# Optimization experiments

Hardware: AMD Instinct MI355X
Metric: run time of the kernel (lower is better)

Reference implementation:

```python
import jax, jax.numpy as jnp
import numpy as np

B, N, H = 32, 1024, 128
EPS = 1e-5


def setup_inputs() -> dict:
    key = jax.random.key(0)
    ks = jax.random.split(key, 9)
    node_embeddings = jax.random.normal(ks[0], (B, N, H), dtype=jnp.float32)
    edge_relations = jax.random.normal(ks[1], (B, N, N, 3), dtype=jnp.float32)
    adjacency = jax.random.randint(ks[2], (N, N), 0, 2, dtype=jnp.int32)
    s_msg = 1.0 / np.sqrt(H + 3)
    s_upd = 1.0 / np.sqrt(2 * H)
    W_msg = jax.random.uniform(ks[3], (H, H + 3), jnp.float32, -s_msg, s_msg)
    b_msg = jax.random.uniform(ks[4], (H,), jnp.float32, -s_msg, s_msg)
    W_upd = jax.random.uniform(ks[5], (H, 2 * H), jnp.float32, -s_upd, s_upd)
    b_upd = jax.random.uniform(ks[6], (H,), jnp.float32, -s_upd, s_upd)
    gamma = jnp.ones((H,), jnp.float32)
    beta = jnp.zeros((H,), jnp.float32)
    return {"node_embeddings": node_embeddings, "edge_relations": edge_relations,
            "adjacency": adjacency, "W_msg": W_msg, "b_msg": b_msg,
            "W_upd": W_upd, "b_upd": b_upd, "gamma": gamma, "beta": beta}


def reference(node_embeddings, edge_relations, adjacency, W_msg, b_msg, W_upd, b_upd, gamma, beta):
    # node_embeddings: [B,N,H]; edge_relations: [B,N,N,3]; adjacency: [N,N]
    b_, n_, h_ = node_embeddings.shape
    mask = (adjacency > 0).astype(node_embeddings.dtype)  # mask[j,i]=1 if i is neighbor of j
    # Split msg_nn weight: Linear(cat(h_i, e_ij)) = h_i @ W_h^T + e_ij @ W_e^T + b
    W_h = W_msg[:, :h_]   # [H,H]
    W_e = W_msg[:, h_:]   # [H,3]
    h_part = jnp.einsum('bih,oh->bio', node_embeddings, W_h)       # [B,N,H]
    msg_h = jnp.einsum('ji,bio->bjo', mask, h_part)                # aggregate sender linear part
    e_agg = jnp.einsum('bijc,ji->bjc', edge_relations, mask)       # aggregate edge feats first (memory-bound)
    msg_e = jnp.einsum('bjc,oc->bjo', e_agg, W_e)
    deg = mask.sum(axis=1)                                         # [N] in-degree of j
    messages = msg_h + msg_e + deg[None, :, None] * b_msg          # bias added once per edge
    # Dropout(0.2) is identity in inference; BatchNorm uses batch stats (training-mode math).
    upd_in = jnp.concatenate([node_embeddings, messages], axis=-1)  # [B,N,2H]
    updated = jax.nn.relu(jnp.einsum('bjk,ok->bjo', upd_in, W_upd) + b_upd)
    flat = updated.reshape(-1, h_)
    mean = flat.mean(axis=0)
    var = flat.var(axis=0)  # biased, as BatchNorm1d
    normed = (flat - mean) * jax.lax.rsqrt(var + EPS) * gamma + beta
    return normed.reshape(b_, n_, h_) + node_embeddings
```

## Files before the change

### kernel.cpp

```cpp
#include <hip/hip_runtime.h>

typedef _Float16 f16;
typedef f16 f16x4 __attribute__((ext_vector_type(4)));
typedef f16 f16x8 __attribute__((ext_vector_type(8)));
typedef float f32x4 __attribute__((ext_vector_type(4)));

#define BB 32
#define NN 1024
#define HH 128
#define ROWS (BB*NN)
#define EPS 1e-5f

__device__ __forceinline__ f16 f2h(float x) { return (f16)x; }

typedef __attribute__((address_space(1))) const void gv_t;
typedef __attribute__((address_space(3))) void lv_t;
__device__ __forceinline__ void gl_lds16(const void* g, void* l) {
  __builtin_amdgcn_global_load_lds((gv_t*)g, (lv_t*)l, 16, 0, 0);
}

__global__ __launch_bounds__(256) void prep0_k(
    const float* __restrict__ W_msg, const float* __restrict__ W_upd,
    const float* __restrict__ node, const int* __restrict__ adj,
    f16* __restrict__ Wh, f16* __restrict__ Wupd, float* __restrict__ We,
    f16* __restrict__ nodeh, f16* __restrict__ maskf, f16* __restrict__ maskT,
    float* __restrict__ e_agg, float* __restrict__ sums)
{
  const int blk = blockIdx.x, t = threadIdx.x;
  if (blk < 64) {
    const long base = (long)blk*16384 + t;
    #pragma unroll
    for (int p = 0; p < 64; p++) {
      const long idx = base + (long)p*256;
      const float4 v = ((const float4*)node)[idx];
      f16x4 hv; hv[0] = f2h(v.x); hv[1] = f2h(v.y); hv[2] = f2h(v.z); hv[3] = f2h(v.w);
      *(f16x4*)&nodeh[idx << 2] = hv;
    }
  } else if (blk < 128) {
    __shared__ f16 ldsT[128][136];
    const int tt = blk - 64, tj = tt >> 3, ti = tt & 7;
    #pragma unroll
    for (int p = 0; p < 16; p++) {
      const int q = p*256 + t;
      const int row = q >> 5, c4 = (q & 31) << 2;
      const int4 m = *(const int4*)&adj[(long)(tj*128 + row)*NN + ti*128 + c4];
      f16x4 hv;
      hv[0] = (m.x > 0) ? (f16)1.0f : (f16)0.0f;
      hv[1] = (m.y > 0) ? (f16)1.0f : (f16)0.0f;
      hv[2] = (m.z > 0) ? (f16)1.0f : (f16)0.0f;
      hv[3] = (m.w > 0) ? (f16)1.0f : (f16)0.0f;
      *(f16x4*)&maskf[(long)(tj*128 + row)*NN + ti*128 + c4] = hv;
      ldsT[c4 + 0][row] = hv[0];
      ldsT[c4 + 1][row] = hv[1];
      ldsT[c4 + 2][row] = hv[2];
      ldsT[c4 + 3][row] = hv[3];
    }
    __syncthreads();
    #pragma unroll
    for (int p = 0; p < 8; p++) {
      const int q = p*256 + t;
      const int rT = q >> 4, c8 = (q & 15) << 3;
      *(uint4*)&maskT[(long)(ti*128 + rT)*NN + tj*128 + c8] =
          *(const uint4*)&ldsT[rT][c8];
    }
  } else if (blk == 128) {
    for (int idx = t; idx < HH*HH; idx += 256) {
      const int o = idx >> 7, h = idx & 127;
      Wh[idx] = f2h(W_msg[o*131 + h]);
    }
  } else if (blk == 129) {
    for (int idx = t; idx < HH*256; idx += 256)
      Wupd[idx] = f2h(W_upd[idx]);
  } else if (blk == 130) {
    for (int idx = t; idx < HH*3; idx += 256)
      We[idx] = W_msg[(idx/3)*131 + 128 + (idx % 3)];
    if (t < 256) sums[t] = 0.f;
  } else {
    const int base = (blk - 131) * 24576 + t;
    #pragma unroll
    for (int r = 0; r < 96; r++) e_agg[base + r*256] = 0.f;
  }
}

__global__ __launch_bounds__(256) void phaseB_k(
    const f16* __restrict__ nodeh, const float* __restrict__ E,
    const f16* __restrict__ maskT, const f16* __restrict__ Wh,
    const float* __restrict__ b_msg,
    f16* __restrict__ h_part_T, float* __restrict__ e_agg)
{
  __shared__ __align__(16) char smem[24576];
  const int tid = threadIdx.x;

  if (blockIdx.x >= 256) {
    float* Ebuf = (float*)smem;
    const int e  = blockIdx.x - 256;
    const int bb = e >> 6;
    const int r6 = e & 63;
    const int jt = r6 & 3;
    const int ih = r6 >> 2;
    const int j  = (jt << 8) + tid;
    const int i0 = ih << 6;
    const int lane = tid & 63, wv = tid >> 6;
    const float* Eblk = E + (long)bb*3145728 + (long)i0*3072 + (long)(jt << 8)*3;
    float a0 = 0.f, a1 = 0.f, a2 = 0.f;
    for (int ch = 0; ch < 8; ch++) {
      const float* Ech = Eblk + (long)ch*8*3072;
      __syncthreads();
      #pragma unroll
      for (int k = 0; k < 6; k++) {
        const int m = wv*6 + k;
        const int r = m/3;
        const int cb = (m % 3) << 8;
        gl_lds16(Ech + (long)r*3072 + cb + lane*4, Ebuf + m*256);
      }
      float mreg[8];
      #pragma unroll
      for (int v = 0; v < 8; v++)
        mreg[v] = (float)maskT[(long)(i0 + ch*8 + v)*NN + j];
      __syncthreads();
      #pragma unroll
      for (int v = 0; v < 8; v++) {
        const float e0 = Ebuf[v*768 + tid*3];
        const float e1 = Ebuf[v*768 + tid*3 + 1];
        const float e2 = Ebuf[v*768 + tid*3 + 2];
        a0 = fmaf(mreg[v], e0, a0);
        a1 = fmaf(mreg[v], e1, a1);
        a2 = fmaf(mreg[v], e2, a2);
      }
    }
    const long eb = ((long)bb*NN + j)*3;
    atomicAdd(&e_agg[eb],     a0);
    atomicAdd(&e_agg[eb + 1], a1);
    atomicAdd(&e_agg[eb + 2], a2);
    return;
  }

  f16* As = (f16*)smem;
  f16* Bs = (f16*)(smem + 8192);
  const int g  = blockIdx.x;
  const int nt = g & 7, bb = g >> 3;
  const int nbase = nt << 7;
  const int lane = tid & 63, wave = tid >> 6;
  const int wm = (wave & 1) << 6, wn = (wave >> 1) << 6;

  f32x4 acc[2][4], acc2[2][4];
  #pragma unroll
  for (int i = 0; i < 2; i++)
    #pragma unroll
    for (int j = 0; j < 4; j++)
      #pragma unroll
      for (int r = 0; r < 4; r++) { acc[i][j][r] = 0.f; acc2[i][j][r] = 0.f; }

  for (int k0 = 0; k0 < HH; k0 += 32) {
    #pragma unroll
    for (int p = 0; p < 2; p++) {
      const int q = (p << 8) + tid;
      const int row = q >> 2, kp = (q & 3) << 3;
      gl_lds16(&Wh[(long)row*HH + k0 + kp], &As[q << 3]);
      gl_lds16(&nodeh[(long)((bb << 10) + nbase + row)*HH + k0 + kp], &Bs[q << 3]);
    }
    __syncthreads();
    f16x8 af[4], bf[4];
    #pragma unroll
    for (int i = 0; i < 4; i++) {
      af[i] = *(const f16x8*)&As[((wm + (i << 4) + (lane & 15)) << 5) + ((lane >> 4) << 3)];
      bf[i] = *(const f16x8*)&Bs[((wn + (i << 4) + (lane & 15)) << 5) + ((lane >> 4) << 3)];
    }
    #pragma unroll
    for (int i = 0; i < 2; i++)
      #pragma unroll
      for (int j = 0; j < 4; j++) {
        acc[i][j]  = __builtin_amdgcn_mfma_f32_16x16x32_f16(af[i],     bf[j], acc[i][j],  0, 0, 0);
        acc2[i][j] = __builtin_amdgcn_mfma_f32_16x16x32_f16(af[i + 2], bf[j], acc2[i][j], 0, 0, 0);
      }
    __syncthreads();
  }

  f16* out = h_part_T + (long)bb * (HH*NN);
  const int rb = (lane >> 4) << 2, cb = lane & 15;
  #pragma unroll
  for (int i = 0; i < 4; i++)
    #pragma unroll
    for (int r = 0; r < 4; r++) {
      const int gm = wm + (i << 4) + rb + r;
      const float bm = b_msg[gm];
      #pragma unroll
      for (int j = 0; j < 4; j++) {
        const int gn = nbase + wn + (j << 4) + cb;
        const float v = ((i < 2) ? acc[i][j][r] : acc2[i - 2][j][r]) + bm;
        out[(long)gm*NN + gn] = f2h(v);
      }
    }
}

__global__ __launch_bounds__(256) void gemm12_k(
    const f16* __restrict__ maskf, const f16* __restrict__ hp,
    const float* __restrict__ e_agg, const float* __restrict__ We,
    const f16* __restrict__ nodeh, const f16* __restrict__ Wupd,
    const float* __restrict__ b_upd,
    f16* __restrict__ upd, float* __restrict__ sums)
{
  const int mt = blockIdx.x, bb = blockIdx.z;
  const int jb = mt << 7;
  const long rowb = (long)bb*NN + jb;
  __shared__ f16 As[128*32];
  __shared__ f16 Bs[128*32];
  __shared__ __align__(16) char msgs_lds[128*128*2];
  __shared__ float colS[128], colQ[128];
  const int tid = threadIdx.x, lane = tid & 63, wave = tid >> 6;
  const int wm = (wave & 1) << 6, wn = (wave >> 1) << 6;
  if (tid < 128) { colS[tid] = 0.f; colQ[tid] = 0.f; }
  const int rb = (lane >> 4) << 2, cb = lane & 15;

  f32x4 acc[4][4];
  #pragma unroll
  for (int i = 0; i < 4; i++)
    #pragma unroll
    for (int j = 0; j < 4; j++)
      #pragma unroll
      for (int r = 0; r < 4; r++) acc[i][j][r] = 0.f;

  for (int k0 = 0; k0 < NN; k0 += 32) {
    #pragma unroll
    for (int p = 0; p < 2; p++) {
      const int q = (p << 8) + tid;
      const int row = q >> 2, kp = (q & 3) << 3;
      gl_lds16(&maskf[(long)(jb + row)*NN + k0 + kp], &As[q << 3]);
      gl_lds16(&hp[(long)bb*(HH*NN) + (long)row*NN + k0 + kp], &Bs[q << 3]);
    }
    __syncthreads();
    f16x8 af[4], bf[4];
    #pragma unroll
    for (int i = 0; i < 4; i++) {
      af[i] = *(const f16x8*)&As[((wm + (i << 4) + (lane & 15)) << 5) + ((lane >> 4) << 3)];
      bf[i] = *(const f16x8*)&Bs[((wn + (i << 4) + (lane & 15)) << 5) + ((lane >> 4) << 3)];
    }
    #pragma unroll
    for (int i = 0; i < 4; i++)
      #pragma unroll
      for (int j = 0; j < 4; j++)
        acc[i][j] = __builtin_amdgcn_mfma_f32_16x16x32_f16(af[i], bf[j], acc[i][j], 0, 0, 0);
    __syncthreads();
  }

  #pragma unroll
  for (int i = 0; i < 4; i++)
    #pragma unroll
    for (int r = 0; r < 4; r++) {
      const int lrow = wm + (i << 4) + rb + r;
      const long eb = (rowb + lrow)*3;
      const float e0 = e_agg[eb], e1 = e_agg[eb+1], e2 = e_agg[eb+2];
      #pragma unroll
      for (int j = 0; j < 4; j++) {
        const int col = wn + (j << 4) + cb;
        const float v = acc[i][j][r]
                      + e0*We[col*3] + e1*We[col*3+1] + e2*We[col*3+2];
        const int byte = ((lrow << 8) + (col << 1)) ^ ((lrow & 7) << 4);
        *(f16*)(msgs_lds + byte) = f2h(v);
      }
    }
  __syncthreads();

  f32x4 acc2[4][4];
  #pragma unroll
  for (int i = 0; i < 4; i++)
    #pragma unroll
    for (int j = 0; j < 4; j++)
      #pragma unroll
      for (int r = 0; r < 4; r++) acc2[i][j][r] = 0.f;

  for (int k0 = 0; k0 < 256; k0 += 32) {
    const bool fromA = (k0 < HH);
    #pragma unroll
    for (int p = 0; p < 2; p++) {
      const int q = (p << 8) + tid;
      const int row = q >> 2, kp = (q & 3) << 3;
      if (fromA)
        gl_lds16(&nodeh[(rowb + row)*HH + k0 + kp], &As[q << 3]);
      gl_lds16(&Wupd[(long)row*256 + k0 + kp], &Bs[q << 3]);
    }
    __syncthreads();
    f16x8 af[4], bf[4];
    #pragma unroll
    for (int i = 0; i < 4; i++) {
      if (fromA) {
        af[i] = *(const f16x8*)&As[((wm + (i << 4) + (lane & 15)) << 5) + ((lane >> 4) << 3)];
      } else {
        const int lrow = wm + (i << 4) + (lane & 15);
        const int byte = ((lrow << 8) + (((k0 - HH) + ((lane >> 4) << 3)) << 1))
                         ^ ((lrow & 7) << 4);
        af[i] = *(const f16x8*)(msgs_lds + byte);
      }
      bf[i] = *(const f16x8*)&Bs[((wn + (i << 4) + (lane & 15)) << 5) + ((lane >> 4) << 3)];
    }
    #pragma unroll
    for (int i = 0; i < 4; i++)
      #pragma unroll
      for (int j = 0; j < 4; j++)
        acc2[i][j] = __builtin_amdgcn_mfma_f32_16x16x32_f16(af[i], bf[j], acc2[i][j], 0, 0, 0);
    __syncthreads();
  }

  float bup[4], s[4] = {0,0,0,0}, qq[4] = {0,0,0,0};
  #pragma unroll
  for (int j = 0; j < 4; j++) bup[j] = b_upd[wn + (j << 4) + cb];
  #pragma unroll
  for (int i = 0; i < 4; i++)
    #pragma unroll
    for (int r = 0; r < 4; r++) {
      const long gm = rowb + wm + (i << 4) + rb + r;
      #pragma unroll
      for (int j = 0; j < 4; j++) {
        const int gn = wn + (j << 4) + cb;
        const float v = fmaxf(acc2[i][j][r] + bup[j], 0.f);
        upd[gm*HH + gn] = f2h(v);
        s[j] += v; qq[j] += v*v;
      }
    }
  #pragma unroll
  for (int j = 0; j < 4; j++) {
    const int gn = wn + (j << 4) + cb;
    atomicAdd(&colS[gn], s[j]);
    atomicAdd(&colQ[gn], qq[j]);
  }
  __syncthreads();
  if (tid < 128) {
    atomicAdd(&sums[tid],       colS[tid]);
    atomicAdd(&sums[128 + tid], colQ[tid]);
  }
}

__global__ __launch_bounds__(256) void final_k(const f16* __restrict__ upd,
    const float* __restrict__ node, const float* __restrict__ sums,
    const float* __restrict__ gamma, const float* __restrict__ beta,
    float* __restrict__ out)
{
  const long idx = (long)blockIdx.x*256 + threadIdx.x;
  const f16x4 u  = *(const f16x4*)&upd[idx << 2];
  const float4 nd = ((const float4*)node)[idx];
  const int ob = (idx & 31) << 2;
  const float inv = 1.0f/32768.0f;
  float4 res;
  #pragma unroll
  for (int c = 0; c < 4; c++) {
    const float m  = sums[ob + c]*inv;
    const float va = sums[128 + ob + c]*inv - m*m;
    const float sc = rsqrtf(va + EPS)*gamma[ob + c];
    ((float*)&res)[c] = ((float)u[c] - m)*sc + beta[ob + c]
                      + ((const float*)&nd)[c];
  }
  ((float4*)out)[idx] = res;
}

extern "C" void kernel_launch(void* const* d_in, const int* in_sizes, int n_in,
                              void* d_out, int out_size, void* d_ws, size_t ws_size,
                              hipStream_t stream) {
  const float* node  = (const float*)d_in[0];
  const float* E     = (const float*)d_in[1];
  const int*   adj   = (const int*)  d_in[2];
  const float* W_msg = (const float*)d_in[3];
  const float* b_msg = (const float*)d_in[4];
  const float* W_upd = (const float*)d_in[5];
  const float* b_upd = (const float*)d_in[6];
  const float* gamma = (const float*)d_in[7];
  const float* beta  = (const float*)d_in[8];
  float* out = (float*)d_out;

  char* p = (char*)d_ws;
  auto alloc = [&](size_t n) { void* r = (void*)p; p += (n + 255) & ~(size_t)255; return r; };
  f16*   h_part_T = (f16*)  alloc((size_t)BB*HH*NN*2);
  f16*   upd      = (f16*)  alloc((size_t)ROWS*HH*2);
  f16*   nodeh    = (f16*)  alloc((size_t)ROWS*HH*2);
  f16*   maskf    = (f16*)  alloc((size_t)NN*NN*2);
  f16*   maskT    = (f16*)  alloc((size_t)NN*NN*2);
  float* e_agg    = (float*)alloc((size_t)BB*NN*3*4);
  f16*   Wh       = (f16*)  alloc((size_t)HH*HH*2);
  f16*   Wupd     = (f16*)  alloc((size_t)HH*256*2);
  float* We       = (float*)alloc((size_t)HH*3*4);
  float* sums     = (float*)alloc((size_t)256*4);

  prep0_k<<<135, 256, 0, stream>>>(W_msg, W_upd, node, adj,
                                   Wh, Wupd, We, nodeh, maskf, maskT,
                                   e_agg, sums);

  phaseB_k<<<2304, 256, 0, stream>>>(nodeh, E, maskT, Wh, b_msg, h_part_T, e_agg);

  gemm12_k<<<dim3(8, 1, BB), 256, 0, stream>>>(maskf, h_part_T, e_agg, We,
                                               nodeh, Wupd, b_upd, upd, sums);

  final_k<<<4096, 256, 0, stream>>>(upd, node, sums, gamma, beta, out);
}
```

Before: 630.7 us.

## Stream edge features with direct float4 loads instead of LDS staging

The edge-aggregation blocks in phaseB now read edge_relations with per-thread float4 loads straight into registers. This replaces the global-to-LDS staging and the two barriers per chunk. Each thread covers four consecutive floats that can span two destination nodes, so it selects between two mask values per component. Work is re-split into 3072 smaller blocks of 32 rows each, which means more atomics to e_agg, and shared memory shrinks because the LDS buffer is gone.

```diff
diff --git a/kernel.cpp b/kernel.cpp
--- a/kernel.cpp
+++ b/kernel.cpp
@@ -88,50 +88,49 @@
     const float* __restrict__ b_msg,
     f16* __restrict__ h_part_T, float* __restrict__ e_agg)
 {
-  __shared__ __align__(16) char smem[24576];
+  __shared__ __align__(16) char smem[16384];
   const int tid = threadIdx.x;
 
   if (blockIdx.x >= 256) {
-    float* Ebuf = (float*)smem;
-    const int e  = blockIdx.x - 256;
-    const int bb = e >> 6;
-    const int r6 = e & 63;
-    const int jt = r6 & 3;
-    const int ih = r6 >> 2;
-    const int j  = (jt << 8) + tid;
-    const int i0 = ih << 6;
-    const int lane = tid & 63, wv = tid >> 6;
-    const float* Eblk = E + (long)bb*3145728 + (long)i0*3072 + (long)(jt << 8)*3;
-    float a0 = 0.f, a1 = 0.f, a2 = 0.f;
-    for (int ch = 0; ch < 8; ch++) {
-      const float* Ech = Eblk + (long)ch*8*3072;
-      __syncthreads();
-      #pragma unroll
-      for (int k = 0; k < 6; k++) {
-        const int m = wv*6 + k;
-        const int r = m/3;
-        const int cb = (m % 3) << 8;
-        gl_lds16(Ech + (long)r*3072 + cb + lane*4, Ebuf + m*256);
-      }
-      float mreg[8];
+    const int e   = blockIdx.x - 256;
+    const int bb  = e / 96;
+    const int rem = e - bb*96;
+    const int seg = rem >> 5;
+    const int ic  = rem & 31;
+    const int i0  = ic << 5;
+    const int p0  = (seg << 10) + (tid << 2);
+    const int j0  = p0 / 3;
+    const int r   = p0 - j0*3;
+    const bool s1 = (r >= 2);
+    const bool s2 = (r >= 1);
+    const float* Ep = E + (long)bb*3145728 + (long)i0*3072 + p0;
+    const f16*   Mp = maskT + (long)i0*NN + j0;
+    float a0 = 0.f, a1 = 0.f, a2 = 0.f, a3 = 0.f;
+    for (int c8 = 0; c8 < 4; c8++) {
+      float4 ev[8];
+      float m0v[8], m1v[8];
       #pragma unroll
       for (int v = 0; v < 8; v++)
-        mreg[v] = (float)maskT[(long)(i0 + ch*8 + v)*NN + j];
-      __syncthreads();
+        ev[v] = *(const float4*)(Ep + (long)(c8*8 + v)*3072);
       #pragma unroll
       for (int v = 0; v < 8; v++) {
-        const float e0 = Ebuf[v*768 + tid*3];
-        const float e1 = Ebuf[v*768 + tid*3 + 1];
-        const float e2 = Ebuf[v*768 + tid*3 + 2];
-        a0 = fmaf(mreg[v], e0, a0);
-        a1 = fmaf(mreg[v], e1, a1);
-        a2 = fmaf(mreg[v], e2, a2);
-      }
-    }
-    const long eb = ((long)bb*NN + j)*3;
-    atomicAdd(&e_agg[eb],     a0);
-    atomicAdd(&e_agg[eb + 1], a1);
-    atomicAdd(&e_agg[eb + 2], a2);
+        const long moff = (long)(c8*8 + v)*NN;
+        m0v[v] = (float)Mp[moff];
+        m1v[v] = (float)Mp[moff + 1];
+      }
+      #pragma unroll
+      for (int v = 0; v < 8; v++) {
+        a0 = fmaf(m0v[v],              ev[v].x, a0);
+        a1 = fmaf(s1 ? m1v[v] : m0v[v], ev[v].y, a1);
+        a2 = fmaf(s2 ? m1v[v] : m0v[v], ev[v].z, a2);
+        a3 = fmaf(m1v[v],              ev[v].w, a3);
+      }
+    }
+    float* ebp = e_agg + (long)bb*3072 + p0;
+    atomicAdd(ebp,     a0);
+    atomicAdd(ebp + 1, a1);
+    atomicAdd(ebp + 2, a2);
+    atomicAdd(ebp + 3, a3);
     return;
   }
 
@@ -383,7 +382,7 @@
                                    Wh, Wupd, We, nodeh, maskf, maskT,
                                    e_agg, sums);
 
-  phaseB_k<<<2304, 256, 0, stream>>>(nodeh, E, maskT, Wh, b_msg, h_part_T, e_agg);
+  phaseB_k<<<3328, 256, 0, stream>>>(nodeh, E, maskT, Wh, b_msg, h_part_T, e_agg);
 
   gemm12_k<<<dim3(8, 1, BB), 256, 0, stream>>>(maskf, h_part_T, e_agg, We,
                                                nodeh, Wupd, b_upd, upd, sums);
```

Result: no change. 624.8 us (-0.9%).
